# Kernel tuning notes

Measured on AMD Instinct MI355X. Metric: run time of the kernel, lower is better.

## Reference

```python
import jax, jax.numpy as jnp
import numpy as np

E = 1024  # embedding_dim
QD = 1024  # query_dim (also key dim)
VD = 1024  # value_dim
B, S = 4, 2048


def setup_inputs() -> dict:
    key = jax.random.key(0)
    k1, k2, k3, k4, k5, k6, k7, k8 = jax.random.split(key, 8)
    x = jax.random.normal(k1, (B, S, E), dtype=jnp.float32)
    mask = jax.random.randint(k2, (B, S, S), 0, 2, dtype=jnp.int32)
    s = 1.0 / np.sqrt(E)
    Wq = jax.random.uniform(k3, (E, QD), jnp.float32, -s, s)
    bq = jax.random.uniform(k4, (QD,), jnp.float32, -s, s)
    Wk = jax.random.uniform(k5, (E, QD), jnp.float32, -s, s)
    bk = jax.random.uniform(k6, (QD,), jnp.float32, -s, s)
    Wv = jax.random.uniform(k7, (E, VD), jnp.float32, -s, s)
    bv = jax.random.uniform(k8, (VD,), jnp.float32, -s, s)
    return {"x": x, "mask": mask, "Wq": Wq, "bq": bq, "Wk": Wk, "bk": bk, "Wv": Wv, "bv": bv}


def reference(x, mask, Wq, bq, Wk, bk, Wv, bv):
    # projections: [B,S,E] @ [E,D] -> [B,S,D]
    q = jnp.einsum('bse,ed->bsd', x, Wq) + bq
    k = jnp.einsum('bse,ed->bsd', x, Wk) + bk
    v = jnp.einsum('bse,ed->bsd', x, Wv) + bv
    # scores scaled by query_dim (NOT sqrt(query_dim)), per original code
    weights = jnp.einsum('bqd,bkd->bqk', q, k) / QD
    weights = jnp.where(mask == 0, -jnp.inf, weights)
    weights = jax.nn.softmax(weights, axis=-1)
    out = jnp.einsum('bqk,bkd->bqd', weights, v)
    return out
```

## Files before the change

kernel.cpp:

```cpp
#include <hip/hip_runtime.h>
#include <hip/hip_bf16.h>


typedef __bf16 bf16x8 __attribute__((ext_vector_type(8)));
typedef __bf16 bf16x4 __attribute__((ext_vector_type(4)));
typedef float f32x4 __attribute__((ext_vector_type(4)));

#define BM 128
#define BN 128
#define BK 64

__device__ inline void glds16(const __bf16* g, __bf16* l) {
    __builtin_amdgcn_global_load_lds(
        (const __attribute__((address_space(1))) unsigned int*)g,
        (__attribute__((address_space(3))) unsigned int*)l,
        16, 0, 0);
}

template <int EPI>
__global__ __launch_bounds__(256) void gemm_bt(
    const __bf16* __restrict__ A, const __bf16* __restrict__ B,
    float* __restrict__ Cf, __bf16* __restrict__ Cb,
    const float* __restrict__ bias, const int* __restrict__ mask,
    int M, int N, int K, float scale,
    long sA, long sB, long sC, long sM)
{
    A += (long)blockIdx.z * sA;
    B += (long)blockIdx.z * sB;
    if (EPI >= 2) Cf += (long)blockIdx.z * sC;
    if (EPI == 2) mask += (long)blockIdx.z * sM;

    __shared__ __align__(16) char smraw[32768];
    __bf16* smA = (__bf16*)smraw;
    __bf16* smB = smA + BM * BK;
    float* smC = (float*)smraw;

    const int t = threadIdx.x;
    const int w = t >> 6;
    const int l = t & 63;
    const int row0 = blockIdx.x * BM;
    const int col0 = blockIdx.y * BN;
    const int wm = (w >> 1) * 64;
    const int wn = (w & 1) * 64;

    const int srow = l >> 3;
    const int skel = (l & 7) * 8;

    const int lm = l & 15;
    const int lk = (l >> 4) * 8;

    f32x4 acc[4][4];
#pragma unroll
    for (int i = 0; i < 4; i++)
#pragma unroll
        for (int j = 0; j < 4; j++) acc[i][j] = (f32x4){0.f, 0.f, 0.f, 0.f};

    for (int kt = 0; kt < K; kt += BK) {
#pragma unroll
        for (int i = 0; i < 4; i++) {
            const int chunk = i * 4 + w;
            const int r = chunk * 8 + srow;
            glds16(A + (size_t)(row0 + r) * K + kt + skel, &smA[chunk * 512]);
            glds16(B + (size_t)(col0 + r) * K + kt + skel, &smB[chunk * 512]);
        }
        __syncthreads();

#pragma unroll
        for (int ks = 0; ks < 2; ks++) {
            bf16x8 af[4], bg[4];
#pragma unroll
            for (int mt = 0; mt < 4; mt++)
                af[mt] = *(const bf16x8*)&smA[(wm + mt * 16 + lm) * BK + ks * 32 + lk];
#pragma unroll
            for (int nt = 0; nt < 4; nt++)
                bg[nt] = *(const bf16x8*)&smB[(wn + nt * 16 + lm) * BK + ks * 32 + lk];
#pragma unroll
            for (int mt = 0; mt < 4; mt++)
#pragma unroll
                for (int nt = 0; nt < 4; nt++)
                    acc[mt][nt] = __builtin_amdgcn_mfma_f32_16x16x32_bf16(
                        af[mt], bg[nt], acc[mt][nt], 0, 0, 0);
        }
        __syncthreads();
    }

    const int rl = (l >> 4) * 4;
    float breg[4];
    if (EPI <= 1) {
#pragma unroll
        for (int nt = 0; nt < 4; nt++) breg[nt] = bias[col0 + wn + nt * 16 + lm];
    }
#pragma unroll
    for (int mt = 0; mt < 4; mt++) {
#pragma unroll
        for (int nt = 0; nt < 4; nt++)
#pragma unroll
            for (int i = 0; i < 4; i++) {
                const int lr = (w >> 1) * 16 + rl + i;
                const int c  = wn + nt * 16 + lm;
                float v = acc[mt][nt][i];
                if (EPI <= 1) v += breg[nt];
                if (EPI == 2) v *= scale;
                smC[lr * 132 + c] = v;
            }
        __syncthreads();

        if (EPI == 1) {
#pragma unroll
            for (int k = 0; k < 4; k++) {
                const int d  = (t >> 3) + 32 * k;
                const int sc = (t & 7) * 4;
                const int gr = row0 + mt * 16 + (sc & 15) + (sc >> 4) * 64;
                bf16x4 o;
#pragma unroll
                for (int j = 0; j < 4; j++) o[j] = (__bf16)smC[(sc + j) * 132 + d];
                *(bf16x4*)&Cb[(size_t)(gr >> 11) * ((size_t)N * 2048)
                              + (size_t)(col0 + d) * 2048 + (gr & 2047)] = o;
            }
        } else {
#pragma unroll
            for (int k = 0; k < 4; k++) {
                const int lr = (t >> 5) + 8 * k;
                const int c4 = (t & 31) * 4;
                const int gr = row0 + mt * 16 + (lr & 15) + (lr >> 4) * 64;
                const float4 v = *(const float4*)&smC[lr * 132 + c4];
                if (EPI == 0) {
                    bf16x4 o = {(__bf16)v.x, (__bf16)v.y, (__bf16)v.z, (__bf16)v.w};
                    *(bf16x4*)&Cb[(size_t)gr * N + col0 + c4] = o;
                } else if (EPI == 2) {
                    const int4 mk = *(const int4*)&mask[(size_t)gr * N + col0 + c4];
                    float4 o;
                    o.x = mk.x ? v.x : -1e30f;
                    o.y = mk.y ? v.y : -1e30f;
                    o.z = mk.z ? v.z : -1e30f;
                    o.w = mk.w ? v.w : -1e30f;
                    *(float4*)&Cf[(size_t)gr * N + col0 + c4] = o;
                } else {
                    *(float4*)&Cf[(size_t)gr * N + col0 + c4] = v;
                }
            }
        }
        __syncthreads();
    }
}

__global__ __launch_bounds__(256) void cast_x(const float* __restrict__ X, __bf16* __restrict__ Y) {
    const size_t i = (size_t)blockIdx.x * 256 + threadIdx.x;
    const float4* X4 = (const float4*)X;
    const float4 a = X4[i * 2], b = X4[i * 2 + 1];
    bf16x8 o = {(__bf16)a.x, (__bf16)a.y, (__bf16)a.z, (__bf16)a.w,
                (__bf16)b.x, (__bf16)b.y, (__bf16)b.z, (__bf16)b.w};
    ((bf16x8*)Y)[i] = o;
}

__global__ void cast_wt(const float* __restrict__ Wq, const float* __restrict__ Wk,
                        const float* __restrict__ Wv, __bf16* __restrict__ Wt) {
    const float* W = blockIdx.z == 0 ? Wq : (blockIdx.z == 1 ? Wk : Wv);
    __bf16* O = Wt + (size_t)blockIdx.z * 1024 * 1024;
    __shared__ float tile[32][33];
    const int tx = threadIdx.x, ty = threadIdx.y;
    const int d0 = blockIdx.x * 32, e0 = blockIdx.y * 32;
#pragma unroll
    for (int j = 0; j < 32; j += 8)
        tile[ty + j][tx] = W[(size_t)(e0 + ty + j) * 1024 + d0 + tx];
    __syncthreads();
#pragma unroll
    for (int j = 0; j < 32; j += 8)
        O[(size_t)(d0 + ty + j) * 1024 + e0 + tx] = (__bf16)tile[tx][ty + j];
}

__global__ __launch_bounds__(256) void softmax_rows(const float* __restrict__ S,
                                                    __bf16* __restrict__ P) {
    const size_t row = blockIdx.x;
    const float4* s4 = (const float4*)(S + row * 2048);
    const int t = threadIdx.x;
    const int w = t >> 6, l = t & 63;
    const float4 a = s4[t * 2], b = s4[t * 2 + 1];
    float v[8] = {a.x, a.y, a.z, a.w, b.x, b.y, b.z, b.w};
    float m = v[0];
#pragma unroll
    for (int i = 1; i < 8; i++) m = fmaxf(m, v[i]);
#pragma unroll
    for (int off = 32; off; off >>= 1) m = fmaxf(m, __shfl_xor(m, off, 64));
    __shared__ float rm[4], rs[4];
    if (l == 0) rm[w] = m;
    __syncthreads();
    m = fmaxf(fmaxf(rm[0], rm[1]), fmaxf(rm[2], rm[3]));
    float e[8], sum = 0.f;
#pragma unroll
    for (int i = 0; i < 8; i++) { e[i] = __expf(v[i] - m); sum += e[i]; }
#pragma unroll
    for (int off = 32; off; off >>= 1) sum += __shfl_xor(sum, off, 64);
    if (l == 0) rs[w] = sum;
    __syncthreads();
    const float inv = 1.f / (rs[0] + rs[1] + rs[2] + rs[3]);
    bf16x8 o;
#pragma unroll
    for (int i = 0; i < 8; i++) o[i] = (__bf16)(e[i] * inv);
    ((bf16x8*)(P + row * 2048))[t] = o;
}

extern "C" void kernel_launch(void* const* d_in, const int* in_sizes, int n_in,
                              void* d_out, int out_size, void* d_ws, size_t ws_size,
                              hipStream_t stream) {
    const float* x  = (const float*)d_in[0];
    const int* mask = (const int*)d_in[1];
    const float* Wq = (const float*)d_in[2];
    const float* bq = (const float*)d_in[3];
    const float* Wk = (const float*)d_in[4];
    const float* bk = (const float*)d_in[5];
    const float* Wv = (const float*)d_in[6];
    const float* bv = (const float*)d_in[7];
    float* out = (float*)d_out;

    char* ws = (char*)d_ws;
    __bf16* xb = (__bf16*)(ws);
    __bf16* Wt = (__bf16*)(ws + (16ull << 20));
    __bf16* Qb = (__bf16*)(ws + (22ull << 20));
    __bf16* Kb = (__bf16*)(ws + (38ull << 20));
    __bf16* Vt = (__bf16*)(ws + (54ull << 20));
    float*  Sf = (float*) (ws + (70ull << 20));
    __bf16* Pb = (__bf16*)(ws + (22ull << 20));

    cast_x<<<4096, 256, 0, stream>>>(x, xb);
    cast_wt<<<dim3(32, 32, 3), dim3(32, 8), 0, stream>>>(Wq, Wk, Wv, Wt);

    gemm_bt<0><<<dim3(64, 8, 1), 256, 0, stream>>>(xb, Wt, nullptr, Qb, bq, nullptr,
                                                   8192, 1024, 1024, 1.f, 0, 0, 0, 0);
    gemm_bt<0><<<dim3(64, 8, 1), 256, 0, stream>>>(xb, Wt + (1u << 20), nullptr, Kb, bk, nullptr,
                                                   8192, 1024, 1024, 1.f, 0, 0, 0, 0);
    gemm_bt<1><<<dim3(64, 8, 1), 256, 0, stream>>>(xb, Wt + (2u << 20), nullptr, Vt, bv, nullptr,
                                                   8192, 1024, 1024, 1.f, 0, 0, 0, 0);

    gemm_bt<2><<<dim3(16, 16, 4), 256, 0, stream>>>(Qb, Kb, Sf, nullptr, nullptr, mask,
                                                    2048, 2048, 1024, 1.0f / 1024.0f,
                                                    2048L * 1024, 2048L * 1024,
                                                    2048L * 2048, 2048L * 2048);

    softmax_rows<<<8192, 256, 0, stream>>>(Sf, Pb);

    gemm_bt<3><<<dim3(16, 8, 4), 256, 0, stream>>>(Pb, Vt, out, nullptr, nullptr, nullptr,
                                                   2048, 1024, 2048, 1.f,
                                                   2048L * 2048, 1024L * 2048,
                                                   2048L * 1024, 0);
}
```

Baseline: 353.8 us.

## Add triple-buffered async LDS pipeline with BK=32 and conflict-free layout

The GEMM main loop now uses three LDS buffers with BK=32. Global-to-LDS loads for two tiles ahead are issued while the current tile feeds MFMA, and a manual vmcnt wait plus barrier replaces the two __syncthreads per iteration. The LDS layout changes so each 16-row group stores its k-chunks contiguously, which is meant to cut bank conflicts on fragment reads. The cost is more LDS (48KB), which may lower occupancy, and the correctness of the hand-written waitcnt counts depends on the exact number of loads issued per stage.

```diff
diff --git a/kernel.cpp b/kernel.cpp
--- a/kernel.cpp
+++ b/kernel.cpp
@@ -8,7 +8,7 @@
 
 #define BM 128
 #define BN 128
-#define BK 64
+#define BK 32
 
 __device__ inline void glds16(const __bf16* g, __bf16* l) {
     __builtin_amdgcn_global_load_lds(
@@ -30,9 +30,7 @@
     if (EPI >= 2) Cf += (long)blockIdx.z * sC;
     if (EPI == 2) mask += (long)blockIdx.z * sM;
 
-    __shared__ __align__(16) char smraw[32768];
-    __bf16* smA = (__bf16*)smraw;
-    __bf16* smB = smA + BM * BK;
+    __shared__ __align__(16) char smraw[49152];
     float* smC = (float*)smraw;
 
     const int t = threadIdx.x;
@@ -43,11 +41,11 @@
     const int wm = (w >> 1) * 64;
     const int wn = (w & 1) * 64;
 
-    const int srow = l >> 3;
-    const int skel = (l & 7) * 8;
+    const int lr16 = l & 15;
+    const int lch  = (l >> 4) * 8;
 
     const int lm = l & 15;
-    const int lk = (l >> 4) * 8;
+    const int g16 = l >> 4;
 
     f32x4 acc[4][4];
 #pragma unroll
@@ -55,34 +53,53 @@
 #pragma unroll
         for (int j = 0; j < 4; j++) acc[i][j] = (f32x4){0.f, 0.f, 0.f, 0.f};
 
-    for (int kt = 0; kt < K; kt += BK) {
-#pragma unroll
-        for (int i = 0; i < 4; i++) {
-            const int chunk = i * 4 + w;
-            const int r = chunk * 8 + srow;
-            glds16(A + (size_t)(row0 + r) * K + kt + skel, &smA[chunk * 512]);
-            glds16(B + (size_t)(col0 + r) * K + kt + skel, &smB[chunk * 512]);
-        }
-        __syncthreads();
-
-#pragma unroll
-        for (int ks = 0; ks < 2; ks++) {
-            bf16x8 af[4], bg[4];
-#pragma unroll
-            for (int mt = 0; mt < 4; mt++)
-                af[mt] = *(const bf16x8*)&smA[(wm + mt * 16 + lm) * BK + ks * 32 + lk];
+    auto stage = [&](int buf, int kt) {
+        __bf16* sA = (__bf16*)(smraw + buf * 16384);
+        __bf16* sB = sA + 4096;
+#pragma unroll
+        for (int j = 0; j < 2; j++) {
+            const int g = j * 4 + w;
+            const int r = g * 16 + lr16;
+            glds16(A + (size_t)(row0 + r) * K + kt + lch, &sA[g * 512]);
+            glds16(B + (size_t)(col0 + r) * K + kt + lch, &sB[g * 512]);
+        }
+    };
+
+    const int n = K / BK;
+    stage(0, 0);
+    stage(1, BK);
+
+    int cur = 0, nxt = 2;
+    for (int i = 0; i < n; i++) {
+        if (i < n - 1) {
+            asm volatile("s_waitcnt vmcnt(4) lgkmcnt(0)\n\ts_barrier" ::: "memory");
+        } else {
+            asm volatile("s_waitcnt vmcnt(0) lgkmcnt(0)\n\ts_barrier" ::: "memory");
+        }
+        if (i + 2 < n) {
+            stage(nxt, (i + 2) * BK);
+        }
+
+        const __bf16* sA = (const __bf16*)(smraw + cur * 16384);
+        const __bf16* sB = sA + 4096;
+        bf16x8 af[4], bg[4];
+#pragma unroll
+        for (int mt = 0; mt < 4; mt++)
+            af[mt] = *(const bf16x8*)&sA[(wm + mt * 16) * 32 + g16 * 128 + lm * 8];
+#pragma unroll
+        for (int nt = 0; nt < 4; nt++)
+            bg[nt] = *(const bf16x8*)&sB[(wn + nt * 16) * 32 + g16 * 128 + lm * 8];
+#pragma unroll
+        for (int mt = 0; mt < 4; mt++)
 #pragma unroll
             for (int nt = 0; nt < 4; nt++)
-                bg[nt] = *(const bf16x8*)&smB[(wn + nt * 16 + lm) * BK + ks * 32 + lk];
-#pragma unroll
-            for (int mt = 0; mt < 4; mt++)
-#pragma unroll
-                for (int nt = 0; nt < 4; nt++)
-                    acc[mt][nt] = __builtin_amdgcn_mfma_f32_16x16x32_bf16(
-                        af[mt], bg[nt], acc[mt][nt], 0, 0, 0);
-        }
-        __syncthreads();
+                acc[mt][nt] = __builtin_amdgcn_mfma_f32_16x16x32_bf16(
+                    af[mt], bg[nt], acc[mt][nt], 0, 0, 0);
+
+        cur = cur == 2 ? 0 : cur + 1;
+        nxt = nxt == 2 ? 0 : nxt + 1;
     }
+    __syncthreads();
 
     const int rl = (l >> 4) * 4;
     float breg[4];
```

Result: slower. 390.6 us (+10.4%).
